# Optimization experiments

Hardware: AMD Instinct MI355X
Metric: run time of the kernel (lower is better)

Reference implementation:

```python
import jax, jax.numpy as jnp
import numpy as np
from jax import lax

B, N, C_IN, C_OUT = 4, 8192, 64, 128
STRIDE, RADIUS, K, L = 4, 0.1, 32, 2
EPS = 1e-5
M = N // STRIDE


def _bn(x, g, b):
    # training-mode batch norm, channel-first layout (B, C, ...)
    axes = (0,) + tuple(range(2, x.ndim))
    mean = jnp.mean(x, axis=axes, keepdims=True)
    var = jnp.mean((x - mean) ** 2, axis=axes, keepdims=True)
    sh = (1, -1) + (1,) * (x.ndim - 2)
    return (x - mean) * lax.rsqrt(var + EPS) * g.reshape(sh) + b.reshape(sh)


def _fps(points, m):
    # farthest point sampling starting at index 0 (matches fps_cuda semantics)
    b, n, _ = points.shape
    bi = jnp.arange(b)

    def body(carry, _):
        dis, last = carry
        lp = points[bi, last]  # (b,3)
        d = jnp.sum((points - lp[:, None, :]) ** 2, -1)
        dis = jnp.minimum(dis, d)
        return (dis, jnp.argmax(dis, -1).astype(jnp.int32)), last

    init = (jnp.full((b, n), 1e10, points.dtype), jnp.zeros((b,), jnp.int32))
    _, idx = lax.scan(body, init, None, length=m)
    return idx.T  # (b, m)


def _ball_query(radius, k, centroids, points, features):
    # first k points within radius of each centroid; pad with first hit
    b, n, _ = points.shape
    d2 = jnp.sum((centroids[:, :, None, :] - points[:, None, :, :]) ** 2, -1)  # (b,m,n)
    key = jnp.where(d2 < radius * radius, jnp.arange(n, dtype=jnp.int32), n)
    neg, _ = lax.top_k(-key, k)  # k smallest keys = first k in-ball indices
    sel = -neg  # (b,m,k)
    sel = jnp.where(sel == n, sel[..., :1], sel)
    sel = jnp.clip(sel, 0, n - 1)
    bi = jnp.arange(b)[:, None, None]
    gp = jnp.transpose(points[bi, sel], (0, 3, 2, 1))  # (b,3,k,m)
    gf = None
    if features is not None:
        gf = jnp.transpose(features[bi, sel], (0, 3, 2, 1))  # (b,c,k,m)
    return gp, gf


def _forward(pos, x, p):
    b, n, _ = pos.shape
    m = n // STRIDE
    bi = jnp.arange(b)[:, None]
    fps_idx = _fps(pos, m)
    centroids = pos[bi, fps_idx]  # (b,m,3)
    # x_mlp: 1x1 conv + BN + ReLU
    f = jax.nn.relu(_bn(jnp.einsum('bnc,oc->bon', x, p['W_x']), p['g_x'], p['b_x']))
    feats = jnp.transpose(f, (0, 2, 1))  # (b,n,C_OUT)
    gp, gf = _ball_query(RADIUS, K, centroids, pos, feats)
    cT = jnp.transpose(centroids, (0, 2, 1))[:, :, None, :]  # (b,3,1,m)
    gp = (gp - cT) / RADIUS
    gp = jax.nn.relu(_bn(jnp.einsum('bckm,oc->bokm', gp, p['W_ps']), p['g_ps'], p['b_ps']))
    xf = jnp.transpose(jnp.max(gf + gp, axis=2), (0, 2, 1))  # (b,m,C_OUT)
    # gen_pe on downsampled points
    R2 = RADIUS * 2
    gpe, _ = _ball_query(R2, K, centroids, centroids, None)
    gpe = (gpe - cT) / R2
    pe = jax.nn.relu(_bn(jnp.einsum('bckm,oc->bokm', gpe, p['W_pe']), p['g_pe'], p['b_pe']))
    # InvResMLP blocks
    for i in range(L):
        xc = jnp.transpose(xf, (0, 2, 1))  # (b,C,m)
        xc = jax.nn.relu(_bn(jnp.einsum('bcm,oc->bom', xc, p['W1'][i]), p['g1'][i], p['b1'][i]))
        feats_i = jnp.transpose(xc, (0, 2, 1))  # (b,m,C)
        _, gfi = _ball_query(R2, K, centroids, centroids, feats_i)
        g = jnp.max(gfi + pe, axis=2)  # (b,C,m)
        g = jax.nn.relu(_bn(jnp.einsum('bcm,oc->bom', g, p['W2a'][i]), p['g2a'][i], p['b2a'][i]))
        g = _bn(jnp.einsum('bcm,oc->bom', g, p['W2b'][i]), p['g2b'][i], p['b2b'][i])
        xf = jax.nn.relu(feats_i + jnp.transpose(g, (0, 2, 1)))
    return centroids, xf


def setup_inputs() -> dict:
    key = jax.random.key(0)
    ks = jax.random.split(key, 12)
    d = {
        'pos': jax.random.uniform(ks[0], (B, N, 3), jnp.float32),
        'x': jax.random.normal(ks[1], (B, N, C_IN), jnp.float32),
        'W_x': jax.random.normal(ks[2], (C_OUT, C_IN), jnp.float32) * 0.05,
        'g_x': jnp.ones((C_OUT,), jnp.float32), 'b_x': jnp.zeros((C_OUT,), jnp.float32),
        'W_ps': jax.random.normal(ks[3], (C_OUT, 3), jnp.float32) * 0.1,
        'g_ps': jnp.ones((C_OUT,), jnp.float32), 'b_ps': jnp.zeros((C_OUT,), jnp.float32),
        'W_pe': jax.random.normal(ks[4], (C_OUT, 3), jnp.float32) * 0.1,
        'g_pe': jnp.ones((C_OUT,), jnp.float32), 'b_pe': jnp.zeros((C_OUT,), jnp.float32),
        'W1': jax.random.normal(ks[5], (L, C_OUT, C_OUT), jnp.float32) * 0.05,
        'g1': jnp.ones((L, C_OUT), jnp.float32), 'b1': jnp.zeros((L, C_OUT), jnp.float32),
        'W2a': jax.random.normal(ks[6], (L, C_OUT, C_OUT), jnp.float32) * 0.05,
        'g2a': jnp.ones((L, C_OUT), jnp.float32), 'b2a': jnp.zeros((L, C_OUT), jnp.float32),
        'W2b': jax.random.normal(ks[7], (L, C_OUT, C_OUT), jnp.float32) * 0.05,
        'g2b': jnp.ones((L, C_OUT), jnp.float32), 'b2b': jnp.zeros((L, C_OUT), jnp.float32),
    }
    return d


def reference(pos, x, W_x, g_x, b_x, W_ps, g_ps, b_ps, W_pe, g_pe, b_pe,
              W1, g1, b1, W2a, g2a, b2a, W2b, g2b, b2b):
    p = dict(W_x=W_x, g_x=g_x, b_x=b_x, W_ps=W_ps, g_ps=g_ps, b_ps=b_ps,
             W_pe=W_pe, g_pe=g_pe, b_pe=b_pe, W1=W1, g1=g1, b1=b1,
             W2a=W2a, g2a=g2a, b2a=b2a, W2b=W2b, g2b=g2b, b2b=b2b)
    return _forward(pos, x, p)
```

## Files before the change

kernel.cpp:

```cpp
#include <hip/hip_runtime.h>


#define BB 4
#define NN 8192
#define MM 2048
#define KK 32
#define CI 64
#define CO 128
#define SG 16

typedef float vf2 __attribute__((ext_vector_type(2)));

#define ST_X 0
#define MO_PS 256
#define MO_PE 272
#define ST1 288
#define ST2A (288 + 2 * SG * 256)
#define ST2B (ST2A + 2 * SG * 256)
#define ST_TOTAL (ST2B + 512)

__device__ __forceinline__ float sq3(float dx, float dy, float dz) {
#pragma clang fp contract(off)
  return dx * dx + dy * dy + dz * dz;
}

__device__ __forceinline__ void fin_stats_d(const double* st, float gam,
                                            float bet, double cnt, int ch,
                                            float* sc, float* sh) {
  double mean = st[ch] / cnt;
  double var = st[128 + ch] / cnt - mean * mean;
  if (var < 0) var = 0;
  double s = (double)gam / sqrt(var + 1e-5);
  *sc = (float)s;
  *sh = (float)((double)bet - mean * s);
}

__device__ __forceinline__ void fin_grp_d(const double* st, float gam,
                                          float bet, double cnt, int ch,
                                          float* sc, float* sh) {
  double sum = 0, ssq = 0;
#pragma unroll
  for (int g = 0; g < SG; g++) {
    sum += st[g * 256 + ch];
    ssq += st[g * 256 + 128 + ch];
  }
  double mean = sum / cnt;
  double var = ssq / cnt - mean * mean;
  if (var < 0) var = 0;
  double s = (double)gam / sqrt(var + 1e-5);
  *sc = (float)s;
  *sh = (float)((double)bet - mean * s);
}

__device__ __forceinline__ void fin_mom_d(const double* mo, const float* Wrow,
                                          float gam, float bet, double cnt,
                                          float* sc, float* sh) {
  double w0 = Wrow[0], w1 = Wrow[1], w2 = Wrow[2];
  double mx = mo[0] / cnt, my = mo[1] / cnt, mz = mo[2] / cnt;
  double sxx = mo[3] / cnt, sxy = mo[4] / cnt, sxz = mo[5] / cnt;
  double syy = mo[6] / cnt, syz = mo[7] / cnt, szz = mo[8] / cnt;
  double mean = w0 * mx + w1 * my + w2 * mz;
  double ey2 = w0 * w0 * sxx + w1 * w1 * syy + w2 * w2 * szz +
               2.0 * (w0 * w1 * sxy + w0 * w2 * sxz + w1 * w2 * syz);
  double var = ey2 - mean * mean;
  if (var < 0) var = 0;
  double s = (double)gam / sqrt(var + 1e-5);
  *sc = (float)s;
  *sh = (float)((double)bet - mean * s);
}

template <int CTRL>
__device__ __forceinline__ int dpp_i(int v) {
  return __builtin_amdgcn_update_dpp(v, v, CTRL, 0xF, 0xF, false);
}
template <int CTRL>
__device__ __forceinline__ float dpp_f(float v) {
  return __int_as_float(dpp_i<CTRL>(__float_as_int(v)));
}

#define FT 512
#define NP 8
#define NW 8

__global__ __launch_bounds__(FT) void k_fps_conv(
    const float* __restrict__ pos, const float* __restrict__ x,
    const float* __restrict__ W_x, float* __restrict__ cent,
    float* __restrict__ fpre, double* __restrict__ stats) {
  __shared__ alignas(16) float s_wv[NW];
  __shared__ alignas(16) int s_wi[NW];
  __shared__ alignas(16) float s_pts[NN * 3];
  __shared__ alignas(16) float s_cent[MM * 3];
  int t = threadIdx.x;
  if (blockIdx.x >= BB) {
    int cb = blockIdx.x - BB;
    int o = t & 127, q = t >> 7;
    float4 w[CI / 4];
    const float4* Wv = (const float4*)(W_x + (size_t)o * CI);
#pragma unroll
    for (int i = 0; i < CI / 4; i++) w[i] = Wv[i];
    int row0 = cb * 128;
    float ssum = 0.f, ssq = 0.f;
    for (int r = 0; r < 128; r += 4) {
      int row = __builtin_amdgcn_readfirstlane(row0 + r + q);
      const float* xr = x + (size_t)row * CI;
      float acc = 0.f;
#pragma unroll
      for (int i = 0; i < CI / 4; i++) {
        float4 a = *(const float4*)(xr + 4 * i);
        acc += a.x * w[i].x + a.y * w[i].y + a.z * w[i].z + a.w * w[i].w;
      }
      fpre[(size_t)row * CO + o] = acc;
      ssum += acc;
      ssq += acc * acc;
    }
    atomicAdd(&stats[ST_X + o], (double)ssum);
    atomicAdd(&stats[ST_X + 128 + o], (double)ssq);
    return;
  }
  int b = blockIdx.x;
  const float* P = pos + (size_t)b * NN * 3;
  float* C = cent + (size_t)b * MM * 3;
  int lane = t & 63, w = t >> 6;
  for (int i = t; i < (NN * 3) / 4; i += FT) {
    ((float4*)s_pts)[i] = ((const float4*)P)[i];
  }
  vf2 px[NP], py[NP], pz[NP], ds[NP];
#pragma unroll
  for (int s = 0; s < NP; s++) {
    int ia = (2 * s) * FT + t;
    int ib = ia + FT;
    px[s] = (vf2){P[ia * 3 + 0], P[ib * 3 + 0]};
    py[s] = (vf2){P[ia * 3 + 1], P[ib * 3 + 1]};
    pz[s] = (vf2){P[ia * 3 + 2], P[ib * 3 + 2]};
    ds[s] = (vf2){1e10f, 1e10f};
  }
  float lx = P[0], ly = P[1], lz = P[2];
  if (t == 0) {
    s_cent[0] = lx;
    s_cent[1] = ly;
    s_cent[2] = lz;
  }
  __syncthreads();
  for (int m = 1; m < MM; m++) {
    vf2 l2x = (vf2){lx, lx}, l2y = (vf2){ly, ly}, l2z = (vf2){lz, lz};
    vf2 bmax = (vf2){-1.0f, -1.0f};
    {
#pragma clang fp contract(off)
#pragma unroll
      for (int s = 0; s < NP; s++) {
        vf2 dx = px[s] - l2x;
        vf2 dy = py[s] - l2y;
        vf2 dz = pz[s] - l2z;
        vf2 d2 = dx * dx + dy * dy + dz * dz;
        vf2 nd = __builtin_elementwise_min(ds[s], d2);
        ds[s] = nd;
        bmax = __builtin_elementwise_max(bmax, nd);
      }
    }
    float bv = fmaxf(bmax.x, bmax.y);
    bv = fmaxf(bv, dpp_f<0x111>(bv));
    bv = fmaxf(bv, dpp_f<0x112>(bv));
    bv = fmaxf(bv, dpp_f<0x114>(bv));
    bv = fmaxf(bv, dpp_f<0x118>(bv));
    bv = fmaxf(bv, dpp_f<0x142>(bv));
    bv = fmaxf(bv, dpp_f<0x143>(bv));
    if (lane == 63) s_wv[w] = bv;
    float gw63 =
        __int_as_float(__builtin_amdgcn_readlane(__float_as_int(bv), 63));
    __syncthreads();
    float4 va = ((const float4*)s_wv)[0];
    float4 vb = ((const float4*)s_wv)[1];
    float gmax = fmaxf(fmaxf(fmaxf(va.x, va.y), fmaxf(va.z, va.w)),
                       fmaxf(fmaxf(vb.x, vb.y), fmaxf(vb.z, vb.w)));
    int bi = 0x7fffffff;
    if (gw63 == gmax) {
#pragma unroll
      for (int s = 0; s < NP; s++) {
        int ia = (2 * s) * FT + t;
        int ib2 = ia + FT;
        bi = (ds[s].x == gmax) ? (ia < bi ? ia : bi) : bi;
        bi = (ds[s].y == gmax) ? (ib2 < bi ? ib2 : bi) : bi;
      }
      int u;
      u = dpp_i<0x111>(bi); bi = u < bi ? u : bi;
      u = dpp_i<0x112>(bi); bi = u < bi ? u : bi;
      u = dpp_i<0x114>(bi); bi = u < bi ? u : bi;
      u = dpp_i<0x118>(bi); bi = u < bi ? u : bi;
      u = dpp_i<0x142>(bi); bi = u < bi ? u : bi;
      u = dpp_i<0x143>(bi); bi = u < bi ? u : bi;
    }
    if (lane == 63) s_wi[w] = bi;
    __syncthreads();
    int4 ia4 = ((const int4*)s_wi)[0];
    int4 ib4 = ((const int4*)s_wi)[1];
    int g0 = ia4.x < ia4.y ? ia4.x : ia4.y;
    int g1 = ia4.z < ia4.w ? ia4.z : ia4.w;
    int g2 = ib4.x < ib4.y ? ib4.x : ib4.y;
    int g3 = ib4.z < ib4.w ? ib4.z : ib4.w;
    g0 = g0 < g1 ? g0 : g1;
    g2 = g2 < g3 ? g2 : g3;
    int gidx = g0 < g2 ? g0 : g2;
    lx = s_pts[gidx * 3 + 0];
    ly = s_pts[gidx * 3 + 1];
    lz = s_pts[gidx * 3 + 2];
    if (t == 0) {
      s_cent[m * 3 + 0] = lx;
      s_cent[m * 3 + 1] = ly;
      s_cent[m * 3 + 2] = lz;
    }
  }
  __syncthreads();
  for (int i = t; i < (MM * 3) / 4; i += FT) {
    ((float4*)C)[i] = ((const float4*)s_cent)[i];
  }
}

__global__ __launch_bounds__(256) void k_bq2(const float* __restrict__ pos,
                                             const float* __restrict__ cent,
                                             int* __restrict__ sel1,
                                             int* __restrict__ sel2,
                                             double* __restrict__ stats) {
  int lane = threadIdx.x & 63, w = threadIdx.x >> 6;
  const float* pts;
  int npts, pair;
  float rsq, inv_r;
  int* sel;
  double* mom;
  int half = (BB * MM) / 4;
  if (blockIdx.x < half) {
    pts = pos; npts = NN; rsq = 0.01f; inv_r = 10.0f;
    sel = sel1; mom = stats + MO_PS;
    pair = blockIdx.x * 4 + w;
  } else {
    pts = cent; npts = MM; rsq = 0.04f; inv_r = 5.0f;
    sel = sel2; mom = stats + MO_PE;
    pair = (blockIdx.x - half) * 4 + w;
  }
  int b = pair / MM;
  const float* P = pts + (size_t)b * npts * 3;
  const float* C = cent + (size_t)pair * 3;
  float cx = C[0], cy = C[1], cz = C[2];
  __shared__ int s_sel[4][KK];
  __shared__ float s_mom[4][9];
  int cnt = 0;
  unsigned long long ltm = (1ull << lane) - 1ull;
  int nit = npts >> 8;
  for (int ch = 0; ch < nit; ch++) {
    int i0 = (ch << 8) + lane;
    bool h0, h1, h2, h3;
    {
      float a0 = P[i0 * 3 + 0], a1 = P[i0 * 3 + 1], a2 = P[i0 * 3 + 2];
      float b0 = P[(i0 + 64) * 3 + 0], b1 = P[(i0 + 64) * 3 + 1],
            b2 = P[(i0 + 64) * 3 + 2];
      float c0 = P[(i0 + 128) * 3 + 0], c1 = P[(i0 + 128) * 3 + 1],
            c2 = P[(i0 + 128) * 3 + 2];
      float e0 = P[(i0 + 192) * 3 + 0], e1 = P[(i0 + 192) * 3 + 1],
            e2 = P[(i0 + 192) * 3 + 2];
      h0 = sq3(a0 - cx, a1 - cy, a2 - cz) < rsq;
      h1 = sq3(b0 - cx, b1 - cy, b2 - cz) < rsq;
      h2 = sq3(c0 - cx, c1 - cy, c2 - cz) < rsq;
      h3 = sq3(e0 - cx, e1 - cy, e2 - cz) < rsq;
    }
    unsigned long long m0 = __ballot(h0);
    unsigned long long m1 = __ballot(h1);
    unsigned long long m2 = __ballot(h2);
    unsigned long long m3 = __ballot(h3);
    if (m0) {
      int k = cnt + __popcll(m0 & ltm);
      if (h0 && k < KK) s_sel[w][k] = i0;
      cnt += __popcll(m0);
    }
    if (m1) {
      int k = cnt + __popcll(m1 & ltm);
      if (h1 && k < KK) s_sel[w][k] = i0 + 64;
      cnt += __popcll(m1);
    }
    if (m2) {
      int k = cnt + __popcll(m2 & ltm);
      if (h2 && k < KK) s_sel[w][k] = i0 + 128;
      cnt += __popcll(m2);
    }
    if (m3) {
      int k = cnt + __popcll(m3 & ltm);
      if (h3 && k < KK) s_sel[w][k] = i0 + 192;
      cnt += __popcll(m3);
    }
    if (cnt >= KK) break;
  }
  int total = cnt < KK ? cnt : KK;
  int myidx = 0;
  if (lane < KK) {
    int v = (lane < total) ? s_sel[w][lane] : s_sel[w][0];
    sel[(size_t)pair * KK + lane] = v;
    myidx = v;
  }
  float gx = 0.f, gy = 0.f, gz = 0.f;
  if (lane < KK) {
    gx = (P[myidx * 3 + 0] - cx) * inv_r;
    gy = (P[myidx * 3 + 1] - cy) * inv_r;
    gz = (P[myidx * 3 + 2] - cz) * inv_r;
  }
  float v9[9] = {gx, gy, gz, gx * gx, gx * gy, gx * gz, gy * gy, gy * gz, gz * gz};
#pragma unroll
  for (int j = 0; j < 9; j++) {
#pragma unroll
    for (int off = 32; off > 0; off >>= 1) v9[j] += __shfl_xor(v9[j], off);
  }
  if (lane == 0) {
#pragma unroll
    for (int j = 0; j < 9; j++) s_mom[w][j] = v9[j];
  }
  __syncthreads();
  if (threadIdx.x < 9) {
    double a = (double)s_mom[0][threadIdx.x] + s_mom[1][threadIdx.x] +
               s_mom[2][threadIdx.x] + s_mom[3][threadIdx.x];
    atomicAdd(&mom[threadIdx.x], a);
  }
}

__global__ __launch_bounds__(128) void k_xf_conv1(
    const float* __restrict__ pos, const float* __restrict__ cent,
    const int* __restrict__ sel1, const float* __restrict__ fpre,
    const float* __restrict__ Wps, const float* __restrict__ g_ps,
    const float* __restrict__ b_ps, const float* __restrict__ g_x,
    const float* __restrict__ b_x, const double* __restrict__ stats,
    const float* __restrict__ W1, float* __restrict__ y1a,
    double* __restrict__ st1out) {
  int pair = blockIdx.x;
  int b = pair >> 11;
  int o = threadIdx.x;
  float sx, hx, sp, hp;
  fin_stats_d(stats + ST_X, g_x[o], b_x[o], (double)(BB * NN), o, &sx, &hx);
  fin_mom_d(stats + MO_PS, Wps + o * 3, g_ps[o], b_ps[o],
            (double)(BB * MM * KK), &sp, &hp);
  float w0 = Wps[o * 3 + 0], w1 = Wps[o * 3 + 1], w2 = Wps[o * 3 + 2];
  const float* C = cent + (size_t)pair * 3;
  float cx = C[0], cy = C[1], cz = C[2];
  const float* P = pos + (size_t)b * NN * 3;
  const float* F = fpre + (size_t)b * NN * CO;
  __shared__ int s_idx[KK];
  __shared__ float s_xf[128];
  if (o < KK) s_idx[o] = sel1[(size_t)pair * KK + o];
  __syncthreads();
  float acc = -1e30f;
#pragma unroll 4
  for (int k = 0; k < KK; k++) {
    int idx = __builtin_amdgcn_readfirstlane(s_idx[k]);
    float gx = (P[idx * 3 + 0] - cx) * 10.0f;
    float gy = (P[idx * 3 + 1] - cy) * 10.0f;
    float gz = (P[idx * 3 + 2] - cz) * 10.0f;
    float y = fmaxf((w0 * gx + w1 * gy + w2 * gz) * sp + hp, 0.f);
    float f = fmaxf(F[(size_t)idx * CO + o] * sx + hx, 0.f);
    float v = y + f;
    acc = v > acc ? v : acc;
  }
  s_xf[o] = acc;
  __syncthreads();
  const float4* Wv = (const float4*)(W1 + (size_t)o * CO);
  const float4* gv = (const float4*)s_xf;
  float dot = 0.f;
#pragma unroll
  for (int i = 0; i < CO / 4; i++) {
    float4 a = gv[i];
    float4 ww = Wv[i];
    dot += a.x * ww.x + a.y * ww.y + a.z * ww.z + a.w * ww.w;
  }
  y1a[(size_t)pair * CO + o] = dot;
  int grp = pair & (SG - 1);
  atomicAdd(&st1out[grp * 256 + o], (double)dot);
  atomicAdd(&st1out[grp * 256 + 128 + o], (double)(dot * dot));
}

__global__ __launch_bounds__(256) void k_conv_bnin(
    const float* __restrict__ in, const float* __restrict__ W,
    const double* __restrict__ st_grp, const float* __restrict__ gam,
    const float* __restrict__ bet, float* __restrict__ out,
    double* __restrict__ stats, int rows_per_block) {
  __shared__ float s_sc[128], s_sh[128];
  int t = threadIdx.x;
  if (t < 128) {
    fin_grp_d(st_grp, gam[t], bet[t], (double)(BB * MM), t, &s_sc[t],
              &s_sh[t]);
  }
  __syncthreads();
  int o = t & 127, half = t >> 7;
  float4 w[CO / 4];
  const float4* Wv = (const float4*)(W + (size_t)o * CO);
#pragma unroll
  for (int i = 0; i < CO / 4; i++) w[i] = Wv[i];
  int row0 = blockIdx.x * rows_per_block;
  float ssum = 0.f, ssq = 0.f;
  for (int r = 0; r < rows_per_block; r += 2) {
    int row = __builtin_amdgcn_readfirstlane(row0 + r + half);
    const float* xr = in + (size_t)row * CO;
    float acc = 0.f;
#pragma unroll
    for (int i = 0; i < CO / 4; i++) {
      float4 a = *(const float4*)(xr + 4 * i);
      a.x = fmaxf(a.x * s_sc[4 * i + 0] + s_sh[4 * i + 0], 0.f);
      a.y = fmaxf(a.y * s_sc[4 * i + 1] + s_sh[4 * i + 1], 0.f);
      a.z = fmaxf(a.z * s_sc[4 * i + 2] + s_sh[4 * i + 2], 0.f);
      a.w = fmaxf(a.w * s_sc[4 * i + 3] + s_sh[4 * i + 3], 0.f);
      acc += a.x * w[i].x + a.y * w[i].y + a.z * w[i].z + a.w * w[i].w;
    }
    out[(size_t)row * CO + o] = acc;
    ssum += acc;
    ssq += acc * acc;
  }
  atomicAdd(&stats[o], (double)ssum);
  atomicAdd(&stats[128 + o], (double)ssq);
}

__global__ __launch_bounds__(256) void k_conv_resid(
    const float* __restrict__ y1prev, const float* __restrict__ y2bprev,
    const double* __restrict__ st1p, const float* __restrict__ g1p,
    const float* __restrict__ b1p, const double* __restrict__ st2bp,
    const float* __restrict__ g2bp, const float* __restrict__ b2bp,
    const float* __restrict__ W, float* __restrict__ y1out,
    double* __restrict__ stats, int rows_per_block) {
  __shared__ float s_s1[128], s_h1[128], s_s2[128], s_h2[128];
  int t = threadIdx.x;
  if (t < 128) {
    fin_grp_d(st1p, g1p[t], b1p[t], (double)(BB * MM), t, &s_s1[t], &s_h1[t]);
    fin_stats_d(st2bp, g2bp[t], b2bp[t], (double)(BB * MM), t, &s_s2[t],
                &s_h2[t]);
  }
  __syncthreads();
  int o = t & 127, half = t >> 7;
  float4 w[CO / 4];
  const float4* Wv = (const float4*)(W + (size_t)o * CO);
#pragma unroll
  for (int i = 0; i < CO / 4; i++) w[i] = Wv[i];
  int row0 = blockIdx.x * rows_per_block;
  float ssum = 0.f, ssq = 0.f;
  for (int r = 0; r < rows_per_block; r += 2) {
    int row = __builtin_amdgcn_readfirstlane(row0 + r + half);
    const float* ar = y1prev + (size_t)row * CO;
    const float* br = y2bprev + (size_t)row * CO;
    float acc = 0.f;
#pragma unroll
    for (int i = 0; i < CO / 4; i++) {
      float4 a = *(const float4*)(ar + 4 * i);
      float4 bb = *(const float4*)(br + 4 * i);
      float x0 = fmaxf(fmaxf(a.x * s_s1[4 * i + 0] + s_h1[4 * i + 0], 0.f) +
                           (bb.x * s_s2[4 * i + 0] + s_h2[4 * i + 0]), 0.f);
      float x1 = fmaxf(fmaxf(a.y * s_s1[4 * i + 1] + s_h1[4 * i + 1], 0.f) +
                           (bb.y * s_s2[4 * i + 1] + s_h2[4 * i + 1]), 0.f);
      float x2 = fmaxf(fmaxf(a.z * s_s1[4 * i + 2] + s_h1[4 * i + 2], 0.f) +
                           (bb.z * s_s2[4 * i + 2] + s_h2[4 * i + 2]), 0.f);
      float x3 = fmaxf(fmaxf(a.w * s_s1[4 * i + 3] + s_h1[4 * i + 3], 0.f) +
                           (bb.w * s_s2[4 * i + 3] + s_h2[4 * i + 3]), 0.f);
      acc += x0 * w[i].x + x1 * w[i].y + x2 * w[i].z + x3 * w[i].w;
    }
    y1out[(size_t)row * CO + o] = acc;
    ssum += acc;
    ssq += acc * acc;
  }
  int grp = blockIdx.x & (SG - 1);
  atomicAdd(&stats[grp * 256 + o], (double)ssum);
  atomicAdd(&stats[grp * 256 + 128 + o], (double)ssq);
}

__global__ __launch_bounds__(128) void k_gconv(
    const float* __restrict__ cent, const int* __restrict__ sel2,
    const float* __restrict__ y1in, const double* __restrict__ st1,
    const float* __restrict__ g1v, const float* __restrict__ b1v,
    const double* __restrict__ mo_pe, const float* __restrict__ Wpe,
    const float* __restrict__ gpe, const float* __restrict__ bpe,
    const float* __restrict__ W2a, float* __restrict__ y2a,
    double* __restrict__ st2a) {
  int pair = blockIdx.x;
  int b = pair >> 11;
  int o = threadIdx.x;
  float s1, h1, se, he;
  fin_grp_d(st1, g1v[o], b1v[o], (double)(BB * MM), o, &s1, &h1);
  fin_mom_d(mo_pe, Wpe + o * 3, gpe[o], bpe[o], (double)(BB * MM * KK), &se,
            &he);
  float w0 = Wpe[o * 3 + 0], w1 = Wpe[o * 3 + 1], w2 = Wpe[o * 3 + 2];
  const float* C = cent + (size_t)pair * 3;
  float cx = C[0], cy = C[1], cz = C[2];
  const float* CB = cent + (size_t)b * MM * 3;
  const float* Y = y1in + (size_t)b * MM * CO;
  __shared__ int s_idx[KK];
  __shared__ float s_g[128];
  if (o < KK) s_idx[o] = sel2[(size_t)pair * KK + o];
  __syncthreads();
  float acc = -1e30f;
#pragma unroll 4
  for (int k = 0; k < KK; k++) {
    int idx = __builtin_amdgcn_readfirstlane(s_idx[k]);
    float gx = (CB[idx * 3 + 0] - cx) * 5.0f;
    float gy = (CB[idx * 3 + 1] - cy) * 5.0f;
    float gz = (CB[idx * 3 + 2] - cz) * 5.0f;
    float pe = fmaxf((w0 * gx + w1 * gy + w2 * gz) * se + he, 0.f);
    float f = fmaxf(Y[(size_t)idx * CO + o] * s1 + h1, 0.f);
    float v = pe + f;
    acc = v > acc ? v : acc;
  }
  s_g[o] = acc;
  __syncthreads();
  const float4* Wv = (const float4*)(W2a + (size_t)o * CO);
  const float4* gv = (const float4*)s_g;
  float dot = 0.f;
#pragma unroll
  for (int i = 0; i < CO / 4; i++) {
    float4 a = gv[i];
    float4 ww = Wv[i];
    dot += a.x * ww.x + a.y * ww.y + a.z * ww.z + a.w * ww.w;
  }
  y2a[(size_t)pair * CO + o] = dot;
  int grp = pair & (SG - 1);
  atomicAdd(&st2a[grp * 256 + o], (double)dot);
  atomicAdd(&st2a[grp * 256 + 128 + o], (double)(dot * dot));
}

__global__ __launch_bounds__(256) void k_resid_fin(
    const float* __restrict__ y1b, const double* __restrict__ st1,
    const float* __restrict__ g1v, const float* __restrict__ b1v,
    const float* __restrict__ y2b, const double* __restrict__ st2b,
    const float* __restrict__ g2bv, const float* __restrict__ b2bv,
    float* __restrict__ xf) {
  int i = blockIdx.x * 256 + threadIdx.x;
  int o = i & 127;
  float s1, h1, s2, h2;
  fin_grp_d(st1, g1v[o], b1v[o], (double)(BB * MM), o, &s1, &h1);
  fin_stats_d(st2b, g2bv[o], b2bv[o], (double)(BB * MM), o, &s2, &h2);
  float f = fmaxf(y1b[i] * s1 + h1, 0.f);
  float v = y2b[i] * s2 + h2;
  xf[i] = fmaxf(f + v, 0.f);
}

extern "C" void kernel_launch(void* const* d_in, const int* in_sizes, int n_in,
                              void* d_out, int out_size, void* d_ws,
                              size_t ws_size, hipStream_t stream) {
  const float* pos = (const float*)d_in[0];
  const float* x = (const float*)d_in[1];
  const float* W_x = (const float*)d_in[2];
  const float* g_x = (const float*)d_in[3];
  const float* b_x = (const float*)d_in[4];
  const float* W_ps = (const float*)d_in[5];
  const float* g_ps = (const float*)d_in[6];
  const float* b_ps = (const float*)d_in[7];
  const float* W_pe = (const float*)d_in[8];
  const float* g_pe = (const float*)d_in[9];
  const float* b_pe = (const float*)d_in[10];
  const float* W1 = (const float*)d_in[11];
  const float* g1 = (const float*)d_in[12];
  const float* b1 = (const float*)d_in[13];
  const float* W2a = (const float*)d_in[14];
  const float* g2a = (const float*)d_in[15];
  const float* b2a = (const float*)d_in[16];
  const float* W2b = (const float*)d_in[17];
  const float* g2b = (const float*)d_in[18];
  const float* b2b = (const float*)d_in[19];

  float* cent = (float*)d_out;
  float* xf = cent + (size_t)BB * MM * 3;

  char* p = (char*)d_ws;
  double* stats = (double*)p; p += (size_t)ST_TOTAL * sizeof(double);
  int* sel1 = (int*)p;        p += (size_t)BB * MM * KK * sizeof(int);
  int* sel2 = (int*)p;        p += (size_t)BB * MM * KK * sizeof(int);
  float* fpre = (float*)p;    p += (size_t)BB * NN * CO * sizeof(float);
  float* y1a = (float*)p;     p += (size_t)BB * MM * CO * sizeof(float);
  float* y1b = (float*)p;     p += (size_t)BB * MM * CO * sizeof(float);
  float* y2a = (float*)p;     p += (size_t)BB * MM * CO * sizeof(float);
  float* y2b = (float*)p;     p += (size_t)BB * MM * CO * sizeof(float);

  hipMemsetAsync(stats, 0, (size_t)ST_TOTAL * sizeof(double), stream);
  k_fps_conv<<<BB + 256, FT, 0, stream>>>(pos, x, W_x, cent, fpre, stats);
  k_bq2<<<(BB * MM) / 2, 256, 0, stream>>>(pos, cent, sel1, sel2, stats);
  k_xf_conv1<<<BB * MM, 128, 0, stream>>>(pos, cent, sel1, fpre, W_ps, g_ps,
                                          b_ps, g_x, b_x, stats, W1, y1a,
                                          stats + ST1);
  k_gconv<<<BB * MM, 128, 0, stream>>>(cent, sel2, y1a, stats + ST1, g1, b1,
                                       stats + MO_PE, W_pe, g_pe, b_pe, W2a,
                                       y2a, stats + ST2A);
  k_conv_bnin<<<128, 256, 0, stream>>>(y2a, W2b, stats + ST2A, g2a, b2a, y2b,
                                       stats + ST2B, 64);
  k_conv_resid<<<128, 256, 0, stream>>>(
      y1a, y2b, stats + ST1, g1, b1, stats + ST2B, g2b, b2b, W1 + CO * CO, y1b,
      stats + ST1 + SG * 256, 64);
  k_gconv<<<BB * MM, 128, 0, stream>>>(cent, sel2, y1b, stats + ST1 + SG * 256,
                                       g1 + 128, b1 + 128, stats + MO_PE, W_pe,
                                       g_pe, b_pe, W2a + CO * CO, y2a,
                                       stats + ST2A + SG * 256);
  k_conv_bnin<<<128, 256, 0, stream>>>(y2a, W2b + CO * CO,
                                       stats + ST2A + SG * 256, g2a + 128,
                                       b2a + 128, y2b, stats + ST2B + 256, 64);
  k_resid_fin<<<(BB * MM * CO) / 256, 256, 0, stream>>>(
      y1b, stats + ST1 + SG * 256, g1 + 128, b1 + 128, y2b,
      stats + ST2B + 256, g2b + 128, b2b + 128, xf);
}
```

Measured before the change: 2.684 ms.

## Cut FPS argmax to one barrier per iteration with packed value-index keys

```diff
diff --git a/kernel.cpp b/kernel.cpp
--- a/kernel.cpp
+++ b/kernel.cpp
@@ -86,8 +86,10 @@
     const float* __restrict__ pos, const float* __restrict__ x,
     const float* __restrict__ W_x, float* __restrict__ cent,
     float* __restrict__ fpre, double* __restrict__ stats) {
-  __shared__ alignas(16) float s_wv[NW];
-  __shared__ alignas(16) int s_wi[NW];
+  __shared__ alignas(16) unsigned long long s_ckey[2][NW];
+  __shared__ alignas(16) float s_cx[2][NW];
+  __shared__ alignas(16) float s_cy[2][NW];
+  __shared__ alignas(16) float s_cz[2][NW];
   __shared__ alignas(16) float s_pts[NN * 3];
   __shared__ alignas(16) float s_cent[MM * 3];
   int t = threadIdx.x;
@@ -164,45 +166,61 @@
     bv = fmaxf(bv, dpp_f<0x118>(bv));
     bv = fmaxf(bv, dpp_f<0x142>(bv));
     bv = fmaxf(bv, dpp_f<0x143>(bv));
-    if (lane == 63) s_wv[w] = bv;
-    float gw63 =
+    float wmax =
         __int_as_float(__builtin_amdgcn_readlane(__float_as_int(bv), 63));
+    int c[2 * NP];
+#pragma unroll
+    for (int s = 0; s < NP; s++) {
+      int ia = (2 * s) * FT + t;
+      int ib2 = ia + FT;
+      c[2 * s] = (ds[s].x == wmax) ? ia : 0x7fffffff;
+      c[2 * s + 1] = (ds[s].y == wmax) ? ib2 : 0x7fffffff;
+    }
+#pragma unroll
+    for (int stp = NP; stp > 0; stp >>= 1) {
+#pragma unroll
+      for (int j = 0; j < stp; j++) c[j] = c[j] < c[j + stp] ? c[j] : c[j + stp];
+    }
+    int bi = c[0];
+    int u;
+    u = dpp_i<0x111>(bi); bi = u < bi ? u : bi;
+    u = dpp_i<0x112>(bi); bi = u < bi ? u : bi;
+    u = dpp_i<0x114>(bi); bi = u < bi ? u : bi;
+    u = dpp_i<0x118>(bi); bi = u < bi ? u : bi;
+    u = dpp_i<0x142>(bi); bi = u < bi ? u : bi;
+    u = dpp_i<0x143>(bi); bi = u < bi ? u : bi;
+    int pb = m & 1;
+    if (lane == 63) {
+      s_ckey[pb][w] = ((unsigned long long)__float_as_uint(wmax) << 32) |
+                      (unsigned)(~(unsigned)bi);
+      s_cx[pb][w] = s_pts[bi * 3 + 0];
+      s_cy[pb][w] = s_pts[bi * 3 + 1];
+      s_cz[pb][w] = s_pts[bi * 3 + 2];
+    }
     __syncthreads();
-    float4 va = ((const float4*)s_wv)[0];
-    float4 vb = ((const float4*)s_wv)[1];
-    float gmax = fmaxf(fmaxf(fmaxf(va.x, va.y), fmaxf(va.z, va.w)),
-                       fmaxf(fmaxf(vb.x, vb.y), fmaxf(vb.z, vb.w)));
-    int bi = 0x7fffffff;
-    if (gw63 == gmax) {
-#pragma unroll
-      for (int s = 0; s < NP; s++) {
-        int ia = (2 * s) * FT + t;
-        int ib2 = ia + FT;
-        bi = (ds[s].x == gmax) ? (ia < bi ? ia : bi) : bi;
-        bi = (ds[s].y == gmax) ? (ib2 < bi ? ib2 : bi) : bi;
+    unsigned long long k[NW];
+    float X[NW], Y[NW], Z[NW];
+#pragma unroll
+    for (int j = 0; j < NW; j++) {
+      k[j] = s_ckey[pb][j];
+      X[j] = s_cx[pb][j];
+      Y[j] = s_cy[pb][j];
+      Z[j] = s_cz[pb][j];
+    }
+#pragma unroll
+    for (int stp = NW / 2; stp > 0; stp >>= 1) {
+#pragma unroll
+      for (int j = 0; j < stp; j++) {
+        bool wn = k[j + stp] > k[j];
+        k[j] = wn ? k[j + stp] : k[j];
+        X[j] = wn ? X[j + stp] : X[j];
+        Y[j] = wn ? Y[j + stp] : Y[j];
+        Z[j] = wn ? Z[j + stp] : Z[j];
       }
-      int u;
-      u = dpp_i<0x111>(bi); bi = u < bi ? u : bi;
-      u = dpp_i<0x112>(bi); bi = u < bi ? u : bi;
-      u = dpp_i<0x114>(bi); bi = u < bi ? u : bi;
-      u = dpp_i<0x118>(bi); bi = u < bi ? u : bi;
-      u = dpp_i<0x142>(bi); bi = u < bi ? u : bi;
-      u = dpp_i<0x143>(bi); bi = u < bi ? u : bi;
-    }
-    if (lane == 63) s_wi[w] = bi;
-    __syncthreads();
-    int4 ia4 = ((const int4*)s_wi)[0];
-    int4 ib4 = ((const int4*)s_wi)[1];
-    int g0 = ia4.x < ia4.y ? ia4.x : ia4.y;
-    int g1 = ia4.z < ia4.w ? ia4.z : ia4.w;
-    int g2 = ib4.x < ib4.y ? ib4.x : ib4.y;
-    int g3 = ib4.z < ib4.w ? ib4.z : ib4.w;
-    g0 = g0 < g1 ? g0 : g1;
-    g2 = g2 < g3 ? g2 : g3;
-    int gidx = g0 < g2 ? g0 : g2;
-    lx = s_pts[gidx * 3 + 0];
-    ly = s_pts[gidx * 3 + 1];
-    lz = s_pts[gidx * 3 + 2];
+    }
+    lx = X[0];
+    ly = Y[0];
+    lz = Z[0];
     if (t == 0) {
       s_cent[m * 3 + 0] = lx;
       s_cent[m * 3 + 1] = ly;
```

After: 3.977 ms. 48.2% more time.
